# Optimization experiments

Measured on AMD Instinct MI355X. Metric: run time of the kernel, lower is better.

Reference implementation:

```python
import jax, jax.numpy as jnp
import numpy as np

B, N, E, F, H, K, C, G = 64, 2048, 16384, 32, 64, 8, 16, 64


def setup_inputs() -> dict:
    key = jax.random.key(0)
    ks = jax.random.split(key, 10)
    s = lambda fan: 1.0 / np.sqrt(fan)
    return {
        "x": jax.random.normal(ks[0], (B, N, C), jnp.float32),
        "linc": (jax.random.uniform(ks[1], (N, E)) < (8.0 / N)).astype(jnp.float32),
        "rinc": (jax.random.uniform(ks[2], (E, N)) < (8.0 / N)).astype(jnp.float32),
        "ef": jax.random.normal(ks[3], (E, F), jnp.float32),
        "w1": jax.random.uniform(ks[4], (H, F), jnp.float32, -s(F), s(F)),
        "b1": jax.random.uniform(ks[5], (H,), jnp.float32, -s(F), s(F)),
        "w2": jax.random.uniform(ks[6], (K, H), jnp.float32, -s(H), s(H)),
        "b2": jax.random.uniform(ks[7], (K,), jnp.float32, -s(H), s(H)),
        "gcw": jax.random.uniform(ks[8], (G, C * K), jnp.float32, -s(C * K), s(C * K)),
        "gcb": jax.random.uniform(ks[9], (G,), jnp.float32, -s(C * K), s(C * K)),
    }


def reference(x, linc, rinc, ef, w1, b1, w2, b2, gcw, gcb):
    # edge MLP -> per-edge kernel weights [E, K]
    h = jax.nn.relu(ef @ w1.T + b1)
    w = h @ w2.T + b2
    # structurally: y_k = linc @ diag(w[:,k]) @ rinc @ x, without building [K,N,N]
    z = jnp.einsum('en,bnc->bec', rinc, x)                  # gather: node -> edge
    y = jnp.einsum('ne,ek,bec->bnck', linc, w, z)           # scale + scatter: edge -> node
    b = x.shape[0]
    y = y.reshape(b, N, C * K)                              # matches permute(0,2,-1,1).reshape
    out = jax.nn.relu(y @ gcw.T + gcb)                      # [B, N, G]
    return out.reshape(b, -1)
```

## Files before the change

### kernel.cpp

```cpp
#include <hip/hip_runtime.h>
#include <hip/hip_bf16.h>

#define B_ 64
#define N_ 2048
#define E_ 16384
#define F_ 32
#define H_ 64
#define K_ 8
#define C_ 16
#define G_ 64
#define CK 128
#define CAP 120
#define RCAP 72
#define YLD 136
#define BC 1024

typedef __attribute__((ext_vector_type(8))) short bf16x8;
typedef __attribute__((ext_vector_type(8))) unsigned short u16x8;
typedef __attribute__((ext_vector_type(4))) float f32x4;

__device__ inline float bf2f(unsigned short u) {
  union { unsigned int i; float f; } v; v.i = ((unsigned int)u) << 16; return v.f;
}
__device__ inline unsigned short f2bf(float f) {
  union { float f; unsigned int i; } v; v.f = f;
  unsigned int x = v.i;
  return (unsigned short)((x + 0x7fffu + ((x >> 16) & 1u)) >> 16);
}

__global__ __launch_bounds__(256) void xpose_k(
    const float* __restrict__ x, const float* __restrict__ gcw,
    unsigned short* __restrict__ x_t, unsigned short* __restrict__ gcw_bf) {
  int t = threadIdx.x;
  if (blockIdx.x == N_) {
    for (int i = t; i < G_*CK; i += 256) gcw_bf[i] = f2bf(gcw[i]);
    return;
  }
  int n = blockIdx.x;
  int b = t >> 2, c0 = (t & 3) * 4;
  float4 xv = *(const float4*)(x + (size_t)b*(N_*C_) + (size_t)n*C_ + c0);
  ushort4 o;
  o.x = f2bf(xv.x); o.y = f2bf(xv.y); o.z = f2bf(xv.z); o.w = f2bf(xv.w);
  *(ushort4*)&x_t[(size_t)n*BC + 4*t] = o;
}

__global__ __launch_bounds__(256) void edge_mlp_k(
    const float* __restrict__ ef, const float* __restrict__ w1,
    const float* __restrict__ b1, const float* __restrict__ w2,
    const float* __restrict__ b2, float* __restrict__ w_out) {
  __shared__ float s_w1[H_*F_];
  __shared__ float s_w2[K_*H_];
  __shared__ float s_b1[H_];
  __shared__ float s_b2[K_];
  int t = threadIdx.x;
  for (int i = t; i < H_*F_; i += 256) s_w1[i] = w1[i];
  for (int i = t; i < K_*H_; i += 256) s_w2[i] = w2[i];
  if (t < H_) s_b1[t] = b1[t];
  if (t < K_) s_b2[t] = b2[t];
  __syncthreads();
  int e = blockIdx.x*256 + t;
  float efr[F_];
  const float4* efp = (const float4*)(ef + (size_t)e*F_);
  #pragma unroll
  for (int f4 = 0; f4 < F_/4; f4++) {
    float4 v = efp[f4];
    efr[f4*4+0]=v.x; efr[f4*4+1]=v.y; efr[f4*4+2]=v.z; efr[f4*4+3]=v.w;
  }
  float acc[K_];
  #pragma unroll
  for (int k = 0; k < K_; k++) acc[k] = s_b2[k];
  #pragma unroll 4
  for (int h = 0; h < H_; h++) {
    float hv = s_b1[h];
    #pragma unroll
    for (int f = 0; f < F_; f++) hv = fmaf(efr[f], s_w1[h*F_+f], hv);
    hv = fmaxf(hv, 0.f);
    #pragma unroll
    for (int k = 0; k < K_; k++) acc[k] = fmaf(hv, s_w2[k*H_+h], acc[k]);
  }
  #pragma unroll
  for (int k = 0; k < K_; k++) w_out[(size_t)e*K_ + k] = acc[k];
}

__global__ __launch_bounds__(256) void gather_z_k(
    const float* __restrict__ rinc, const unsigned short* __restrict__ x_t,
    unsigned short* __restrict__ z) {
  __shared__ int s_idx[4][RCAP];
  __shared__ int s_cnt[4];
  int t = threadIdx.x, wv = t >> 6, lane = t & 63;
  int e = blockIdx.x * 4 + wv;
  if (lane == 0) s_cnt[wv] = 0;
  const f32x4* row = (const f32x4*)(rinc + (size_t)e*N_);
  #pragma unroll
  for (int j = 0; j < N_/4/64; j++) {
    int i = lane + 64*j;
    f32x4 v = __builtin_nontemporal_load(row + i);
    if (v.x != 0.f) { int p = atomicAdd(&s_cnt[wv],1); if (p<RCAP) s_idx[wv][p]=i*4+0; }
    if (v.y != 0.f) { int p = atomicAdd(&s_cnt[wv],1); if (p<RCAP) s_idx[wv][p]=i*4+1; }
    if (v.z != 0.f) { int p = atomicAdd(&s_cnt[wv],1); if (p<RCAP) s_idx[wv][p]=i*4+2; }
    if (v.w != 0.f) { int p = atomicAdd(&s_cnt[wv],1); if (p<RCAP) s_idx[wv][p]=i*4+3; }
  }
  int cnt = min(s_cnt[wv], RCAP);
  const unsigned short* xb = x_t + 16*lane;
  float acc[16];
  #pragma unroll
  for (int k = 0; k < 16; k++) acc[k] = 0.f;
  for (int i = 0; i < cnt; i++) {
    int n = s_idx[wv][i];
    u16x8 a0 = *(const u16x8*)(xb + (size_t)n*BC);
    u16x8 a1 = *(const u16x8*)(xb + (size_t)n*BC + 8);
    #pragma unroll
    for (int k = 0; k < 8; k++) { acc[k] += bf2f(a0[k]); acc[8+k] += bf2f(a1[k]); }
  }
  u16x8 o0, o1;
  #pragma unroll
  for (int k = 0; k < 8; k++) { o0[k] = f2bf(acc[k]); o1[k] = f2bf(acc[8+k]); }
  unsigned short* zp = z + (size_t)e*BC + 16*lane;
  *(u16x8*)zp = o0;
  *(u16x8*)(zp + 8) = o1;
}

__global__ __launch_bounds__(256, 6) void node_out_k(
    const float* __restrict__ linc, const unsigned short* __restrict__ z,
    const float* __restrict__ w, const unsigned short* __restrict__ gcw_bf,
    const float* __restrict__ gcb, float* __restrict__ out) {
  __shared__ unsigned short s_y[B_*YLD];
  __shared__ unsigned short s_wb[CAP*K_];
  __shared__ float s_gcb[G_];
  __shared__ int   s_idx[CAP];
  __shared__ int   s_cnt;
  int t = threadIdx.x;
  int n = blockIdx.x;
  if (t == 0) s_cnt = 0;
  if (t < G_) s_gcb[t] = gcb[t];
  __syncthreads();

  const f32x4* row = (const f32x4*)(linc + (size_t)n*E_);
  #pragma unroll
  for (int j = 0; j < E_/4/256; j++) {
    int i = t + 256*j;
    f32x4 v = __builtin_nontemporal_load(row + i);
    if (v.x != 0.f) { int p = atomicAdd(&s_cnt,1); if (p<CAP) s_idx[p]=i*4+0; }
    if (v.y != 0.f) { int p = atomicAdd(&s_cnt,1); if (p<CAP) s_idx[p]=i*4+1; }
    if (v.z != 0.f) { int p = atomicAdd(&s_cnt,1); if (p<CAP) s_idx[p]=i*4+2; }
    if (v.w != 0.f) { int p = atomicAdd(&s_cnt,1); if (p<CAP) s_idx[p]=i*4+3; }
  }
  __syncthreads();
  int cnt = min(s_cnt, CAP);
  for (int i = t; i < cnt*K_; i += 256) {
    int ii = i >> 3, k = i & 7;
    s_wb[i] = f2bf(w[(size_t)s_idx[ii]*K_ + k]);
  }
  __syncthreads();

  float acc[4][K_];
  #pragma unroll
  for (int j = 0; j < 4; j++)
    #pragma unroll
    for (int k = 0; k < K_; k++) acc[j][k] = 0.f;
  const unsigned short* zt = z + 4*t;
  for (int i = 0; i < cnt; i++) {
    int e = s_idx[i];
    u16x8 wv8 = *(const u16x8*)&s_wb[i*K_];
    float we[K_];
    #pragma unroll
    for (int k = 0; k < K_; k++) we[k] = bf2f(wv8[k]);
    ushort4 zu = *(const ushort4*)(zt + (size_t)e*BC);
    float zv[4] = {bf2f(zu.x), bf2f(zu.y), bf2f(zu.z), bf2f(zu.w)};
    #pragma unroll
    for (int j = 0; j < 4; j++)
      #pragma unroll
      for (int k = 0; k < K_; k++) acc[j][k] = fmaf(zv[j], we[k], acc[j][k]);
  }
  {
    int b = t >> 2, ckb = (t & 3) * 32;
    #pragma unroll
    for (int j = 0; j < 4; j++) {
      ushort4 lo, hi;
      lo.x = f2bf(acc[j][0]); lo.y = f2bf(acc[j][1]); lo.z = f2bf(acc[j][2]); lo.w = f2bf(acc[j][3]);
      hi.x = f2bf(acc[j][4]); hi.y = f2bf(acc[j][5]); hi.z = f2bf(acc[j][6]); hi.w = f2bf(acc[j][7]);
      *(ushort4*)&s_y[b*YLD + ckb + 8*j]     = lo;
      *(ushort4*)&s_y[b*YLD + ckb + 8*j + 4] = hi;
    }
  }
  __syncthreads();

  {
    int wv = t >> 6, lane = t & 63;
    int m = lane & 15, q = lane >> 4;
    f32x4 cf0 = {0.f,0.f,0.f,0.f}, cf1 = cf0, cf2 = cf0, cf3 = cf0;
    #pragma unroll
    for (int ks = 0; ks < 4; ks++) {
      bf16x8 a = *(const bf16x8*)&s_y[(16*wv + m)*YLD + 32*ks + 8*q];
      bf16x8 b0 = *(const bf16x8*)&gcw_bf[(size_t)(m     )*CK + 32*ks + 8*q];
      bf16x8 b1 = *(const bf16x8*)&gcw_bf[(size_t)(16 + m)*CK + 32*ks + 8*q];
      bf16x8 b2 = *(const bf16x8*)&gcw_bf[(size_t)(32 + m)*CK + 32*ks + 8*q];
      bf16x8 b3 = *(const bf16x8*)&gcw_bf[(size_t)(48 + m)*CK + 32*ks + 8*q];
      cf0 = __builtin_amdgcn_mfma_f32_16x16x32_bf16(a, b0, cf0, 0, 0, 0);
      cf1 = __builtin_amdgcn_mfma_f32_16x16x32_bf16(a, b1, cf1, 0, 0, 0);
      cf2 = __builtin_amdgcn_mfma_f32_16x16x32_bf16(a, b2, cf2, 0, 0, 0);
      cf3 = __builtin_amdgcn_mfma_f32_16x16x32_bf16(a, b3, cf3, 0, 0, 0);
    }
    float* ob = out + (size_t)n*G_;
    #pragma unroll
    for (int r = 0; r < 4; r++) {
      int b = 16*wv + 4*q + r;
      float* op = ob + (size_t)b*(N_*G_);
      float v0 = fmaxf(cf0[r] + s_gcb[m],      0.f);
      float v1 = fmaxf(cf1[r] + s_gcb[16 + m], 0.f);
      float v2 = fmaxf(cf2[r] + s_gcb[32 + m], 0.f);
      float v3 = fmaxf(cf3[r] + s_gcb[48 + m], 0.f);
      op[m]      = v0;
      op[16 + m] = v1;
      op[32 + m] = v2;
      op[48 + m] = v3;
    }
  }
}

extern "C" void kernel_launch(void* const* d_in, const int* in_sizes, int n_in,
                              void* d_out, int out_size, void* d_ws, size_t ws_size,
                              hipStream_t stream) {
  const float* x    = (const float*)d_in[0];
  const float* linc = (const float*)d_in[1];
  const float* rinc = (const float*)d_in[2];
  const float* ef   = (const float*)d_in[3];
  const float* w1   = (const float*)d_in[4];
  const float* b1   = (const float*)d_in[5];
  const float* w2   = (const float*)d_in[6];
  const float* b2   = (const float*)d_in[7];
  const float* gcw  = (const float*)d_in[8];
  const float* gcb  = (const float*)d_in[9];
  float* out = (float*)d_out;

  char* ws = (char*)d_ws;
  float* w_e             = (float*)ws;            ws += (size_t)E_*K_*sizeof(float);
  unsigned short* z      = (unsigned short*)ws;   ws += (size_t)E_*BC*sizeof(short);
  unsigned short* x_t    = (unsigned short*)ws;   ws += (size_t)N_*BC*sizeof(short);
  unsigned short* gcw_bf = (unsigned short*)ws;   ws += (size_t)G_*CK*sizeof(short);

  xpose_k<<<N_+1, 256, 0, stream>>>(x, gcw, x_t, gcw_bf);
  edge_mlp_k<<<E_/256, 256, 0, stream>>>(ef, w1, b1, w2, b2, w_e);
  gather_z_k<<<E_/4, 256, 0, stream>>>(rinc, x_t, z);
  node_out_k<<<N_, 256, 0, stream>>>(linc, z, w_e, gcw_bf, gcb, out);
}
```

Baseline: 369.9 us.

## Precompute sparse incidence index lists in a dedicated scan kernel

Adds a scan kernel that streams the dense linc and rinc incidence matrices once. It writes compacted 16-bit nonzero index lists and counts to workspace, using global atomics on per-row counters that are zeroed in the transpose kernel. The gather and node-output kernels now read these short lists instead of scanning full dense rows inline. The gather kernel distributes indices with wave shuffles, and RCAP drops to 32. Node output keeps edge weights as fp32 in shared memory instead of bf16. This separates the bandwidth-bound scan from the compute and gather phases at the cost of an extra launch, global atomics and index writes.

```diff
diff --git a/kernel.cpp b/kernel.cpp
--- a/kernel.cpp
+++ b/kernel.cpp
@@ -11,7 +11,7 @@
 #define G_ 64
 #define CK 128
 #define CAP 120
-#define RCAP 72
+#define RCAP 32
 #define YLD 136
 #define BC 1024
 
@@ -30,18 +30,62 @@
 
 __global__ __launch_bounds__(256) void xpose_k(
     const float* __restrict__ x, const float* __restrict__ gcw,
-    unsigned short* __restrict__ x_t, unsigned short* __restrict__ gcw_bf) {
-  int t = threadIdx.x;
-  if (blockIdx.x == N_) {
-    for (int i = t; i < G_*CK; i += 256) gcw_bf[i] = f2bf(gcw[i]);
+    unsigned short* __restrict__ x_t, unsigned short* __restrict__ gcw_bf,
+    int* __restrict__ cnts ) {
+  int t = threadIdx.x;
+  int blk = blockIdx.x;
+  if (blk >= N_) {
+    if (blk == N_) {
+      for (int i = t; i < G_*CK; i += 256) gcw_bf[i] = f2bf(gcw[i]);
+    } else {
+      int zid = blk - (N_ + 1);
+      for (int i = zid*256 + t; i < N_ + E_; i += 8*256) cnts[i] = 0;
+    }
     return;
   }
-  int n = blockIdx.x;
+  int n = blk;
   int b = t >> 2, c0 = (t & 3) * 4;
   float4 xv = *(const float4*)(x + (size_t)b*(N_*C_) + (size_t)n*C_ + c0);
   ushort4 o;
   o.x = f2bf(xv.x); o.y = f2bf(xv.y); o.z = f2bf(xv.z); o.w = f2bf(xv.w);
   *(ushort4*)&x_t[(size_t)n*BC + 4*t] = o;
+}
+
+__global__ __launch_bounds__(256) void scan_k(
+    const float* __restrict__ linc, const float* __restrict__ rinc,
+    int* __restrict__ lcnt, unsigned short* __restrict__ lidx,
+    int* __restrict__ rcnt, unsigned short* __restrict__ ridx) {
+  int t = threadIdx.x;
+  int blk = blockIdx.x;
+  if (blk < N_) {
+    int n = blk;
+    const f32x4* row = (const f32x4*)(linc + (size_t)n*E_);
+    unsigned short* lrow = lidx + (size_t)n*CAP;
+    #pragma unroll
+    for (int j = 0; j < E_/4/256; j++) {
+      int i = t + 256*j;
+      f32x4 v = __builtin_nontemporal_load(row + i);
+      if (v.x != 0.f) { int p = atomicAdd(&lcnt[n],1); if (p<CAP) lrow[p] = (unsigned short)(i*4+0); }
+      if (v.y != 0.f) { int p = atomicAdd(&lcnt[n],1); if (p<CAP) lrow[p] = (unsigned short)(i*4+1); }
+      if (v.z != 0.f) { int p = atomicAdd(&lcnt[n],1); if (p<CAP) lrow[p] = (unsigned short)(i*4+2); }
+      if (v.w != 0.f) { int p = atomicAdd(&lcnt[n],1); if (p<CAP) lrow[p] = (unsigned short)(i*4+3); }
+    }
+  } else {
+    int e0 = (blk - N_) * 8;
+    const f32x4* base = (const f32x4*)(rinc + (size_t)e0*N_);
+    #pragma unroll
+    for (int j = 0; j < 8*N_/4/256; j++) {
+      int i = t + 256*j;
+      f32x4 v = __builtin_nontemporal_load(base + i);
+      int e = e0 + (i >> 9);
+      int nn = (i & 511) * 4;
+      unsigned short* rrow = ridx + (size_t)e*RCAP;
+      if (v.x != 0.f) { int p = atomicAdd(&rcnt[e],1); if (p<RCAP) rrow[p] = (unsigned short)(nn+0); }
+      if (v.y != 0.f) { int p = atomicAdd(&rcnt[e],1); if (p<RCAP) rrow[p] = (unsigned short)(nn+1); }
+      if (v.z != 0.f) { int p = atomicAdd(&rcnt[e],1); if (p<RCAP) rrow[p] = (unsigned short)(nn+2); }
+      if (v.w != 0.f) { int p = atomicAdd(&rcnt[e],1); if (p<RCAP) rrow[p] = (unsigned short)(nn+3); }
+    }
+  }
 }
 
 __global__ __launch_bounds__(256) void edge_mlp_k(
@@ -83,30 +127,19 @@
 }
 
 __global__ __launch_bounds__(256) void gather_z_k(
-    const float* __restrict__ rinc, const unsigned short* __restrict__ x_t,
-    unsigned short* __restrict__ z) {
-  __shared__ int s_idx[4][RCAP];
-  __shared__ int s_cnt[4];
+    const int* __restrict__ rcnt, const unsigned short* __restrict__ ridx,
+    const unsigned short* __restrict__ x_t, unsigned short* __restrict__ z) {
   int t = threadIdx.x, wv = t >> 6, lane = t & 63;
   int e = blockIdx.x * 4 + wv;
-  if (lane == 0) s_cnt[wv] = 0;
-  const f32x4* row = (const f32x4*)(rinc + (size_t)e*N_);
-  #pragma unroll
-  for (int j = 0; j < N_/4/64; j++) {
-    int i = lane + 64*j;
-    f32x4 v = __builtin_nontemporal_load(row + i);
-    if (v.x != 0.f) { int p = atomicAdd(&s_cnt[wv],1); if (p<RCAP) s_idx[wv][p]=i*4+0; }
-    if (v.y != 0.f) { int p = atomicAdd(&s_cnt[wv],1); if (p<RCAP) s_idx[wv][p]=i*4+1; }
-    if (v.z != 0.f) { int p = atomicAdd(&s_cnt[wv],1); if (p<RCAP) s_idx[wv][p]=i*4+2; }
-    if (v.w != 0.f) { int p = atomicAdd(&s_cnt[wv],1); if (p<RCAP) s_idx[wv][p]=i*4+3; }
-  }
-  int cnt = min(s_cnt[wv], RCAP);
+  int cnt = min(rcnt[e], RCAP);
+  int my = 0;
+  if (lane < cnt) my = ridx[(size_t)e*RCAP + lane];
   const unsigned short* xb = x_t + 16*lane;
   float acc[16];
   #pragma unroll
   for (int k = 0; k < 16; k++) acc[k] = 0.f;
   for (int i = 0; i < cnt; i++) {
-    int n = s_idx[wv][i];
+    int n = __shfl(my, i);
     u16x8 a0 = *(const u16x8*)(xb + (size_t)n*BC);
     u16x8 a1 = *(const u16x8*)(xb + (size_t)n*BC + 8);
     #pragma unroll
@@ -121,36 +154,23 @@
 }
 
 __global__ __launch_bounds__(256, 6) void node_out_k(
-    const float* __restrict__ linc, const unsigned short* __restrict__ z,
-    const float* __restrict__ w, const unsigned short* __restrict__ gcw_bf,
-    const float* __restrict__ gcb, float* __restrict__ out) {
+    const int* __restrict__ lcnt, const unsigned short* __restrict__ lidx,
+    const unsigned short* __restrict__ z, const float* __restrict__ w,
+    const unsigned short* __restrict__ gcw_bf, const float* __restrict__ gcb,
+    float* __restrict__ out) {
   __shared__ unsigned short s_y[B_*YLD];
-  __shared__ unsigned short s_wb[CAP*K_];
+  __shared__ float s_w[CAP*K_];
   __shared__ float s_gcb[G_];
   __shared__ int   s_idx[CAP];
-  __shared__ int   s_cnt;
   int t = threadIdx.x;
   int n = blockIdx.x;
-  if (t == 0) s_cnt = 0;
   if (t < G_) s_gcb[t] = gcb[t];
-  __syncthreads();
-
-  const f32x4* row = (const f32x4*)(linc + (size_t)n*E_);
-  #pragma unroll
-  for (int j = 0; j < E_/4/256; j++) {
-    int i = t + 256*j;
-    f32x4 v = __builtin_nontemporal_load(row + i);
-    if (v.x != 0.f) { int p = atomicAdd(&s_cnt,1); if (p<CAP) s_idx[p]=i*4+0; }
-    if (v.y != 0.f) { int p = atomicAdd(&s_cnt,1); if (p<CAP) s_idx[p]=i*4+1; }
-    if (v.z != 0.f) { int p = atomicAdd(&s_cnt,1); if (p<CAP) s_idx[p]=i*4+2; }
-    if (v.w != 0.f) { int p = atomicAdd(&s_cnt,1); if (p<CAP) s_idx[p]=i*4+3; }
-  }
-  __syncthreads();
-  int cnt = min(s_cnt, CAP);
-  for (int i = t; i < cnt*K_; i += 256) {
-    int ii = i >> 3, k = i & 7;
-    s_wb[i] = f2bf(w[(size_t)s_idx[ii]*K_ + k]);
-  }
+
+  int cnt = min(lcnt[n], CAP);
+  const unsigned short* lrow = lidx + (size_t)n*CAP;
+  for (int i = t; i < cnt; i += 256) s_idx[i] = lrow[i];
+  for (int i = t; i < cnt*K_; i += 256)
+    s_w[i] = w[(size_t)lrow[i >> 3]*K_ + (i & 7)];
   __syncthreads();
 
   float acc[4][K_];
@@ -161,10 +181,9 @@
   const unsigned short* zt = z + 4*t;
   for (int i = 0; i < cnt; i++) {
     int e = s_idx[i];
-    u16x8 wv8 = *(const u16x8*)&s_wb[i*K_];
-    float we[K_];
-    #pragma unroll
-    for (int k = 0; k < K_; k++) we[k] = bf2f(wv8[k]);
+    const float4* wp = (const float4*)&s_w[i*K_];
+    float4 w0 = wp[0], w1v = wp[1];
+    float we[K_] = {w0.x, w0.y, w0.z, w0.w, w1v.x, w1v.y, w1v.z, w1v.w};
     ushort4 zu = *(const ushort4*)(zt + (size_t)e*BC);
     float zv[4] = {bf2f(zu.x), bf2f(zu.y), bf2f(zu.z), bf2f(zu.w)};
     #pragma unroll
@@ -238,9 +257,14 @@
   unsigned short* z      = (unsigned short*)ws;   ws += (size_t)E_*BC*sizeof(short);
   unsigned short* x_t    = (unsigned short*)ws;   ws += (size_t)N_*BC*sizeof(short);
   unsigned short* gcw_bf = (unsigned short*)ws;   ws += (size_t)G_*CK*sizeof(short);
-
-  xpose_k<<<N_+1, 256, 0, stream>>>(x, gcw, x_t, gcw_bf);
+  int* lcnt              = (int*)ws;              ws += (size_t)N_*sizeof(int);
+  int* rcnt              = (int*)ws;              ws += (size_t)E_*sizeof(int);
+  unsigned short* lidx   = (unsigned short*)ws;   ws += (size_t)N_*CAP*sizeof(short);
+  unsigned short* ridx   = (unsigned short*)ws;   ws += (size_t)E_*RCAP*sizeof(short);
+
+  xpose_k<<<N_ + 1 + 8, 256, 0, stream>>>(x, gcw, x_t, gcw_bf, lcnt);
+  scan_k<<<N_ + E_/8, 256, 0, stream>>>(linc, rinc, lcnt, lidx, rcnt, ridx);
   edge_mlp_k<<<E_/256, 256, 0, stream>>>(ef, w1, b1, w2, b2, w_e);
-  gather_z_k<<<E_/4, 256, 0, stream>>>(rinc, x_t, z);
-  node_out_k<<<N_, 256, 0, stream>>>(linc, z, w_e, gcw_bf, gcb, out);
-}
+  gather_z_k<<<E_/4, 256, 0, stream>>>(rcnt, ridx, x_t, z);
+  node_out_k<<<N_, 256, 0, stream>>>(lcnt, lidx, z, w_e, gcw_bf, gcb, out);
+}
```

Result: slower. 393.5 us (+6.4%).
